# Optimization experiments

Hardware: AMD Instinct MI355X
Metric: run time of the kernel (lower is better)

## Reference

```python
import jax, jax.numpy as jnp
import numpy as np

D = 256
K = 3  # depthwise conv kernel size (odd)
A_EPS = 1e-4
POW_MIN = 1e-20
LN_EPS = 1e-5


def setup_inputs() -> dict:
    key = jax.random.key(0)
    ks = jax.random.split(key, 10)
    B, H, W = 8, 96, 96
    x = jax.random.normal(ks[0], (B, H, W, D), dtype=jnp.float32)
    inp = {
        'x': x,
        'ln_g': jnp.ones((D,), jnp.float32),
        'ln_b': jnp.zeros((D,), jnp.float32),
        'w_in': jax.random.normal(ks[1], (D, 2 * D), jnp.float32) * 0.02,
        'b_in': jnp.zeros((2 * D,), jnp.float32),
        'conv_w': jax.random.normal(ks[2], (K, K, 1, D), jnp.float32) * 0.1,
        'conv_b': jnp.zeros((D,), jnp.float32),
        'a_logit': 7.0 + 0.1 * jax.random.normal(ks[3], (D,), jnp.float32),
        'ssm_b': jnp.ones((D,), jnp.float32) + 0.02 * jax.random.normal(ks[4], (D,), jnp.float32),
        'ssm_c': jnp.ones((D,), jnp.float32) + 0.02 * jax.random.normal(ks[5], (D,), jnp.float32),
        'ssm_d': jnp.ones((D,), jnp.float32) + 0.02 * jax.random.normal(ks[6], (D,), jnp.float32),
        'w_out': jax.random.normal(ks[7], (D, D), jnp.float32) * 0.02,
        'b_out': jnp.zeros((D,), jnp.float32),
    }
    return inp


def _ssm_scan(x, a_logit, b, c, d):
    # x: (N, L, D). s_t = a*s_{t-1} + b*x_t ; y_t = c*s_t + d*x_t
    # via log-domain cumsum reformulation (as in the torch source).
    L = x.shape[1]
    a = jnp.clip(jax.nn.sigmoid(a_logit), A_EPS, 1.0 - A_EPS)  # (D,)
    t = jnp.arange(L, dtype=jnp.float32)
    a_pow = jnp.maximum(jnp.exp(t[:, None] * jnp.log(a)[None, :]), POW_MIN)  # (L,D)
    u = x * b  # (N,L,D)
    r = jnp.cumsum(u / a_pow[None], axis=1)
    return r * a_pow[None] * c + x * d


def reference(x, ln_g, ln_b, w_in, b_in, conv_w, conv_b,
              a_logit, ssm_b, ssm_c, ssm_d, w_out, b_out):
    B, H, W, Dm = x.shape
    x0 = x
    # LayerNorm over channel dim
    mu = jnp.mean(x, axis=-1, keepdims=True)
    var = jnp.mean(jnp.square(x - mu), axis=-1, keepdims=True)
    h = (x - mu) * jax.lax.rsqrt(var + LN_EPS) * ln_g + ln_b
    # in_proj -> split into value and gate
    xg = h @ w_in + b_in  # (B,H,W,2D)
    x_in, gate = jnp.split(xg, 2, axis=-1)
    gate = jax.nn.sigmoid(gate)
    # depthwise conv (SAME padding) + SiLU, NHWC layout
    u = jax.lax.conv_general_dilated(
        x_in, conv_w, window_strides=(1, 1), padding='SAME',
        dimension_numbers=('NHWC', 'HWIO', 'NHWC'), feature_group_count=Dm)
    u = jax.nn.silu(u + conv_b)
    # 2D bidirectional scan mixing
    L = H * W
    seq_row = u.reshape(B, L, Dm)
    seq_col = u.transpose(0, 2, 1, 3).reshape(B, L, Dm)

    def bid(s):
        yf = _ssm_scan(s, a_logit, ssm_b, ssm_c, ssm_d)
        yb = jnp.flip(_ssm_scan(jnp.flip(s, axis=1), a_logit, ssm_b, ssm_c, ssm_d), axis=1)
        return 0.5 * (yf + yb)

    y_row = bid(seq_row).reshape(B, H, W, Dm)
    y_col = bid(seq_col).reshape(B, W, H, Dm).transpose(0, 2, 1, 3)
    y = 0.5 * (y_row + y_col)
    # gate, out_proj, residual
    y = y * gate
    y = y @ w_out + b_out
    return x0 + y
```

## Files before the change

### kernel.cpp

```cpp
#include <hip/hip_runtime.h>
#include <math.h>

#define DD   256
#define HHH  96
#define WWW  96
#define NB   8
#define LL   9216
#define NPIX (NB*LL)
#define TCH  32
#define NCH  (LL/TCH)

typedef __bf16 bf16_8 __attribute__((ext_vector_type(8)));
typedef float  f32_4  __attribute__((ext_vector_type(4)));

static __device__ __forceinline__ float sigmoidf_(float x) {
    return 1.0f / (1.0f + expf(-x));
}

typedef const __attribute__((address_space(1))) void gas_void;
typedef __attribute__((address_space(3))) void las_void;
static __device__ __forceinline__ void glld16(const void* g, void* l) {
    __builtin_amdgcn_global_load_lds((gas_void*)g, (las_void*)l, 16, 0, 0);
}

template<int DIR>
static __device__ __forceinline__ int spidx(int t) {
    if (DIR == 0) return t;
    int w = t / HHH;
    int h = t - w * HHH;
    return h * WWW + w;
}

__global__ __launch_bounds__(256) void wcvt_kernel(const float* __restrict__ w_in,
                                                   const float* __restrict__ w_out,
                                                   __bf16* __restrict__ w_inT,
                                                   __bf16* __restrict__ w_outT) {
    int i = blockIdx.x * 256 + threadIdx.x;
    int n = i >> 8, k = i & 255;
    w_inT[i] = (__bf16)w_in[k * 512 + n];
    if (i < 256 * 256) w_outT[i] = (__bf16)w_out[k * 256 + n];
}

__global__ __launch_bounds__(256) void ln_kernel(const float* __restrict__ x,
                                                 const float* __restrict__ g,
                                                 const float* __restrict__ b,
                                                 __bf16* __restrict__ h) {
    int wv = threadIdx.x >> 6, lane = threadIdx.x & 63;
    int pix = blockIdx.x * 4 + wv;
    const float4 v = *(const float4*)&x[(size_t)pix * DD + lane * 4];
    float s  = v.x + v.y + v.z + v.w;
    float s2 = v.x * v.x + v.y * v.y + v.z * v.z + v.w * v.w;
    #pragma unroll
    for (int o = 32; o > 0; o >>= 1) {
        s  += __shfl_xor(s, o, 64);
        s2 += __shfl_xor(s2, o, 64);
    }
    float mu  = s * (1.0f / 256.0f);
    float var = s2 * (1.0f / 256.0f) - mu * mu;
    float r = rsqrtf(var + 1e-5f);
    float4 gg = *(const float4*)&g[lane * 4];
    float4 bb = *(const float4*)&b[lane * 4];
    union { ushort4 u; __bf16 e[4]; } o4;
    o4.e[0] = (__bf16)((v.x - mu) * r * gg.x + bb.x);
    o4.e[1] = (__bf16)((v.y - mu) * r * gg.y + bb.y);
    o4.e[2] = (__bf16)((v.z - mu) * r * gg.z + bb.z);
    o4.e[3] = (__bf16)((v.w - mu) * r * gg.w + bb.w);
    *(ushort4*)&h[(size_t)pix * DD + lane * 4] = o4.u;
}

template<int MODE>
__global__ __launch_bounds__(256) void gemm_bf16(const __bf16* __restrict__ A,
                                                 const __bf16* __restrict__ BT,
                                                 const float* __restrict__ bias,
                                                 __bf16* __restrict__ out_xin,
                                                 __bf16* __restrict__ out_gate,
                                                 float* __restrict__ out_f32,
                                                 const float* __restrict__ x0) {
    const int K = 256;
    const int BK = 32;
    __shared__ __bf16 As[2][128 * BK];
    __shared__ __bf16 Bs[2][128 * BK];
    int tid = threadIdx.x;
    int lane = tid & 63, wv = tid >> 6;
    int rowBase = blockIdx.x * 128;
    int colBase = blockIdx.y * 128;

    int srow = tid >> 2, sseg = tid & 3;
    const __bf16* aS0 = A  + (size_t)(rowBase + srow) * K + sseg * 8;
    const __bf16* aS1 = A  + (size_t)(rowBase + srow + 64) * K + sseg * 8;
    const __bf16* bS0 = BT + (size_t)(colBase + srow) * K + sseg * 8;
    const __bf16* bS1 = BT + (size_t)(colBase + srow + 64) * K + sseg * 8;
    int wvoff = wv * 1024;

    int m0 = (wv >> 1) * 64, n0 = (wv & 1) * 64;
    int fr = lane & 15, fq = lane >> 4;

    f32_4 acc[4][4];
    #pragma unroll
    for (int i = 0; i < 4; i++)
        #pragma unroll
        for (int j = 0; j < 4; j++) acc[i][j] = (f32_4){0.f, 0.f, 0.f, 0.f};

#define STAGE(bufi, koff)                                                  \
    do {                                                                   \
        glld16(aS0 + (koff), (char*)&As[bufi][0] + wvoff);                 \
        glld16(aS1 + (koff), (char*)&As[bufi][0] + 4096 + wvoff);          \
        glld16(bS0 + (koff), (char*)&Bs[bufi][0] + wvoff);                 \
        glld16(bS1 + (koff), (char*)&Bs[bufi][0] + 4096 + wvoff);          \
    } while (0)

    STAGE(0, 0);
    __syncthreads();
    int cur = 0;
    for (int t = 0; t < 8; ++t) {
        if (t < 7) STAGE(cur ^ 1, (t + 1) * BK);
        bf16_8 af[4], bb[4];
        #pragma unroll
        for (int mi = 0; mi < 4; mi++)
            af[mi] = *(const bf16_8*)&As[cur][(m0 + mi * 16 + fr) * BK + fq * 8];
        #pragma unroll
        for (int ni = 0; ni < 4; ni++)
            bb[ni] = *(const bf16_8*)&Bs[cur][(n0 + ni * 16 + fr) * BK + fq * 8];
        #pragma unroll
        for (int mi = 0; mi < 4; mi++)
            #pragma unroll
            for (int ni = 0; ni < 4; ni++)
                acc[mi][ni] = __builtin_amdgcn_mfma_f32_16x16x32_bf16(
                    af[mi], bb[ni], acc[mi][ni], 0, 0, 0);
        __syncthreads();
        cur ^= 1;
    }
#undef STAGE

    int rowW = rowBase + m0 + fq * 4;
    int colW = colBase + n0 + fr;
    #pragma unroll
    for (int mi = 0; mi < 4; mi++) {
        #pragma unroll
        for (int ni = 0; ni < 4; ni++) {
            int col = colW + ni * 16;
            float bv = bias[col];
            #pragma unroll
            for (int r = 0; r < 4; r++) {
                int row = rowW + mi * 16 + r;
                float v = acc[mi][ni][r] + bv;
                if (MODE == 0) {
                    if (col < 256) {
                        out_xin[(size_t)row * 256 + col] = (__bf16)v;
                    } else {
                        out_gate[(size_t)row * 256 + (col - 256)] = (__bf16)sigmoidf_(v);
                    }
                } else {
                    out_f32[(size_t)row * 256 + col] = v + x0[(size_t)row * 256 + col];
                }
            }
        }
    }
}

static __device__ __forceinline__ void loadcol(const __bf16* __restrict__ xin,
                                               int b, int h, int w, int d,
                                               float c[3]) {
    if (w < 0 || w >= WWW) { c[0] = c[1] = c[2] = 0.f; return; }
    size_t base = ((size_t)b * LL + (size_t)h * WWW + w) * DD + d;
    c[0] = (h > 0)       ? (float)xin[base - (size_t)WWW * DD] : 0.f;
    c[1] = (float)xin[base];
    c[2] = (h + 1 < HHH) ? (float)xin[base + (size_t)WWW * DD] : 0.f;
}

__global__ __launch_bounds__(256) void conv_tot_kernel(const __bf16* __restrict__ xin,
                                                       const float* __restrict__ cw,
                                                       const float* __restrict__ cb,
                                                       const float* __restrict__ a_logit,
                                                       const float* __restrict__ ssm_b,
                                                       __bf16* __restrict__ u,
                                                       float* __restrict__ tot_f,
                                                       float* __restrict__ tot_b) {
    int cx = blockIdx.x, h = blockIdx.y, b = blockIdx.z;
    int d = threadIdx.x;
    int w0 = cx * TCH;
    float k[9];
    #pragma unroll
    for (int i = 0; i < 9; i++) k[i] = cw[i * DD + d];
    float bias = cb[d];
    float a = sigmoidf_(a_logit[d]);
    a = fminf(fmaxf(a, 1e-4f), 1.0f - 1e-4f);
    float bb = ssm_b[d];

    float cl[3], cc[3], cr[3];
    loadcol(xin, b, h, w0 - 1, d, cl);
    loadcol(xin, b, h, w0,     d, cc);
    loadcol(xin, b, h, w0 + 1, d, cr);

    float v[TCH];
    float sf = 0.f;
    size_t outBase = ((size_t)b * LL + (size_t)h * WWW + w0) * DD + d;
    #pragma unroll
    for (int j = 0; j < TCH; j++) {
        float nx[3];
        loadcol(xin, b, h, w0 + j + 2, d, nx);
        float acc = bias;
        acc += k[0] * cl[0] + k[1] * cc[0] + k[2] * cr[0];
        acc += k[3] * cl[1] + k[4] * cc[1] + k[5] * cr[1];
        acc += k[6] * cl[2] + k[7] * cc[2] + k[8] * cr[2];
        float uv = acc * sigmoidf_(acc);
        v[j] = uv;
        u[outBase + (size_t)j * DD] = (__bf16)uv;
        sf = a * sf + bb * uv;
        cl[0] = cc[0]; cl[1] = cc[1]; cl[2] = cc[2];
        cc[0] = cr[0]; cc[1] = cr[1]; cc[2] = cr[2];
        cr[0] = nx[0]; cr[1] = nx[1]; cr[2] = nx[2];
    }
    int chunk = h * 3 + cx;
    tot_f[((size_t)b * NCH + chunk) * DD + d] = sf;
    float sb = 0.f;
    #pragma unroll
    for (int j = TCH - 1; j >= 0; j--) sb = a * sb + bb * v[j];
    tot_b[((size_t)b * NCH + chunk) * DD + d] = sb;
}

__global__ __launch_bounds__(256) void scan_totals_col(const __bf16* __restrict__ u,
                                                       const float* __restrict__ a_logit,
                                                       const float* __restrict__ ssm_b,
                                                       float* __restrict__ tot_f,
                                                       float* __restrict__ tot_b) {
    int blk = blockIdx.x;
    int b = blk / NCH, c = blk - b * NCH;
    int d = threadIdx.x;
    float a = sigmoidf_(a_logit[d]);
    a = fminf(fmaxf(a, 1e-4f), 1.0f - 1e-4f);
    float bb = ssm_b[d];
    size_t base = (size_t)b * LL * DD;
    int t0 = c * TCH;
    float v[TCH];
    #pragma unroll
    for (int j = 0; j < TCH; j++)
        v[j] = (float)u[base + (size_t)spidx<1>(t0 + j) * DD + d];
    float s = 0.f;
    #pragma unroll
    for (int j = 0; j < TCH; j++) s = a * s + bb * v[j];
    tot_f[(size_t)blk * DD + d] = s;
    s = 0.f;
    #pragma unroll
    for (int j = TCH - 1; j >= 0; j--) s = a * s + bb * v[j];
    tot_b[(size_t)blk * DD + d] = s;
}

__global__ __launch_bounds__(256) void scan_carries(const float* __restrict__ tot_all,
                                                    const float* __restrict__ a_logit,
                                                    float* __restrict__ car_all) {
    int b = blockIdx.x;
    int var = blockIdx.y;
    int d = threadIdx.x;
    float a = sigmoidf_(a_logit[d]);
    a = fminf(fmaxf(a, 1e-4f), 1.0f - 1e-4f);
    float a2 = a * a, a4 = a2 * a2, a8 = a4 * a4, a16 = a8 * a8;
    float q = a16 * a16;
    const float* tot = tot_all + (size_t)var * NB * NCH * DD + (size_t)b * NCH * DD + d;
    float* car = car_all + (size_t)var * NB * NCH * DD + (size_t)b * NCH * DD + d;
    float P = 0.f;
    if ((var & 1) == 0) {
        for (int c0 = 0; c0 < NCH; c0 += 8) {
            float t[8];
            #pragma unroll
            for (int j = 0; j < 8; j++) t[j] = tot[(size_t)(c0 + j) * DD];
            #pragma unroll
            for (int j = 0; j < 8; j++) {
                car[(size_t)(c0 + j) * DD] = P;
                P = q * P + t[j];
            }
        }
    } else {
        for (int c0 = NCH - 8; c0 >= 0; c0 -= 8) {
            float t[8];
            #pragma unroll
            for (int j = 0; j < 8; j++) t[j] = tot[(size_t)(c0 + j) * DD];
            #pragma unroll
            for (int j = 7; j >= 0; j--) {
                car[(size_t)(c0 + j) * DD] = P;
                P = q * P + t[j];
            }
        }
    }
}

template<int DIR>
__global__ __launch_bounds__(256) void scan_apply(const __bf16* __restrict__ u,
                                                  const float* __restrict__ a_logit,
                                                  const float* __restrict__ ssm_b,
                                                  const float* __restrict__ ssm_c,
                                                  const float* __restrict__ ssm_d,
                                                  const float* __restrict__ car_f,
                                                  const float* __restrict__ car_b,
                                                  float* __restrict__ y,
                                                  const __bf16* __restrict__ gate,
                                                  __bf16* __restrict__ g) {
    int blk = blockIdx.x;
    int b = blk / NCH, c = blk - b * NCH;
    int d = threadIdx.x;
    float a = sigmoidf_(a_logit[d]);
    a = fminf(fmaxf(a, 1e-4f), 1.0f - 1e-4f);
    float bb = ssm_b[d], cc = ssm_c[d], dd = ssm_d[d];
    size_t base = (size_t)b * LL * DD;
    int t0 = c * TCH;
    float v[TCH];
    #pragma unroll
    for (int j = 0; j < TCH; j++)
        v[j] = (float)u[base + (size_t)spidx<DIR>(t0 + j) * DD + d];
    float yf[TCH];
    float s = car_f[(size_t)blk * DD + d];
    #pragma unroll
    for (int j = 0; j < TCH; j++) {
        s = a * s + bb * v[j];
        yf[j] = cc * s + dd * v[j];
    }
    s = car_b[(size_t)blk * DD + d];
    #pragma unroll
    for (int j = TCH - 1; j >= 0; j--) {
        s = a * s + bb * v[j];
        float val = 0.25f * (yf[j] + cc * s + dd * v[j]);
        size_t idx = base + (size_t)spidx<DIR>(t0 + j) * DD + d;
        if (DIR == 0) {
            y[idx] = val;
        } else {
            float t = y[idx] + val;
            g[idx] = (__bf16)(t * (float)gate[idx]);
        }
    }
}

extern "C" void kernel_launch(void* const* d_in, const int* in_sizes, int n_in,
                              void* d_out, int out_size, void* d_ws, size_t ws_size,
                              hipStream_t stream) {
    const float* x       = (const float*)d_in[0];
    const float* ln_g    = (const float*)d_in[1];
    const float* ln_b    = (const float*)d_in[2];
    const float* w_in    = (const float*)d_in[3];
    const float* b_in    = (const float*)d_in[4];
    const float* conv_w  = (const float*)d_in[5];
    const float* conv_b  = (const float*)d_in[6];
    const float* a_logit = (const float*)d_in[7];
    const float* ssm_b   = (const float*)d_in[8];
    const float* ssm_c   = (const float*)d_in[9];
    const float* ssm_d   = (const float*)d_in[10];
    const float* w_out   = (const float*)d_in[11];
    const float* b_out   = (const float*)d_in[12];
    float* out = (float*)d_out;

    char* ws = (char*)d_ws;
    const size_t SZH = (size_t)NPIX * DD * sizeof(__bf16);
    const size_t TS  = (size_t)NB * NCH * DD * sizeof(float);

    __bf16* hB     = (__bf16*)(ws);
    __bf16* xinB   = (__bf16*)(ws + SZH);
    __bf16* uB     = (__bf16*)(ws + 2 * SZH);
    __bf16* gateB  = (__bf16*)(ws + 3 * SZH);
    float*  tot    = (float*)(ws + 4 * SZH);
    float*  car    = (float*)(ws + 4 * SZH + 4 * TS);
    __bf16* w_inT  = (__bf16*)(ws + 4 * SZH + 8 * TS);
    __bf16* w_outT = w_inT + 512 * 256;
    float* y = out;

    wcvt_kernel<<<512, 256, 0, stream>>>(w_in, w_out, w_inT, w_outT);
    ln_kernel<<<NPIX / 4, 256, 0, stream>>>(x, ln_g, ln_b, hB);
    gemm_bf16<0><<<dim3(NPIX / 128, 4), 256, 0, stream>>>(hB, w_inT, b_in,
                                                          xinB, gateB, nullptr, nullptr);
    conv_tot_kernel<<<dim3(WWW / TCH, HHH, NB), 256, 0, stream>>>(
        xinB, conv_w, conv_b, a_logit, ssm_b, uB,
        tot + 0 * (size_t)NB * NCH * DD, tot + 1 * (size_t)NB * NCH * DD);
    scan_totals_col<<<NB * NCH, 256, 0, stream>>>(
        uB, a_logit, ssm_b,
        tot + 2 * (size_t)NB * NCH * DD, tot + 3 * (size_t)NB * NCH * DD);
    scan_carries<<<dim3(NB, 4), 256, 0, stream>>>(tot, a_logit, car);
    scan_apply<0><<<NB * NCH, 256, 0, stream>>>(
        uB, a_logit, ssm_b, ssm_c, ssm_d,
        car + 0 * (size_t)NB * NCH * DD, car + 1 * (size_t)NB * NCH * DD,
        y, nullptr, nullptr);
    scan_apply<1><<<NB * NCH, 256, 0, stream>>>(
        uB, a_logit, ssm_b, ssm_c, ssm_d,
        car + 2 * (size_t)NB * NCH * DD, car + 3 * (size_t)NB * NCH * DD,
        y, gateB, hB);
    gemm_bf16<1><<<dim3(NPIX / 128, 2), 256, 0, stream>>>(hB, w_outT, b_out,
                                                          nullptr, nullptr, out, x);
}
```

Baseline: 410.8 us.

## Load full K panel into LDS upfront and prefetch residual in GEMM

The GEMM now issues async global-to-LDS loads for all eight K slices at once (128 KB of LDS), then runs the MFMA loop with one barrier instead of double-buffering with a barrier per slice. For the out-projection mode it also prefetches the residual x0 values into registers before compute so their latency overlaps the matrix math. The cost is far higher LDS use and register pressure, with launch bounds capped at one block per CU, so occupancy drops.

```diff
diff --git a/kernel.cpp b/kernel.cpp
--- a/kernel.cpp
+++ b/kernel.cpp
@@ -69,7 +69,7 @@
 }
 
 template<int MODE>
-__global__ __launch_bounds__(256) void gemm_bf16(const __bf16* __restrict__ A,
+__global__ __launch_bounds__(256, 1) void gemm_bf16(const __bf16* __restrict__ A,
                                                  const __bf16* __restrict__ BT,
                                                  const float* __restrict__ bias,
                                                  __bf16* __restrict__ out_xin,
@@ -78,8 +78,8 @@
                                                  const float* __restrict__ x0) {
     const int K = 256;
     const int BK = 32;
-    __shared__ __bf16 As[2][128 * BK];
-    __shared__ __bf16 Bs[2][128 * BK];
+    __shared__ __bf16 As[8][128 * BK];
+    __shared__ __bf16 Bs[8][128 * BK];
     int tid = threadIdx.x;
     int lane = tid & 63, wv = tid >> 6;
     int rowBase = blockIdx.x * 128;
@@ -94,6 +94,28 @@
 
     int m0 = (wv >> 1) * 64, n0 = (wv & 1) * 64;
     int fr = lane & 15, fq = lane >> 4;
+    int rowW = rowBase + m0 + fq * 4;
+    int colW = colBase + n0 + fr;
+
+    #pragma unroll
+    for (int t = 0; t < 8; ++t) {
+        glld16(aS0 + t * BK, (char*)&As[t][0] + wvoff);
+        glld16(aS1 + t * BK, (char*)&As[t][0] + 4096 + wvoff);
+        glld16(bS0 + t * BK, (char*)&Bs[t][0] + wvoff);
+        glld16(bS1 + t * BK, (char*)&Bs[t][0] + 4096 + wvoff);
+    }
+
+    float x0r[4][4][4];
+    if (MODE == 1) {
+        #pragma unroll
+        for (int mi = 0; mi < 4; mi++)
+            #pragma unroll
+            for (int ni = 0; ni < 4; ni++)
+                #pragma unroll
+                for (int r = 0; r < 4; r++)
+                    x0r[mi][ni][r] = x0[(size_t)(rowW + mi * 16 + r) * 256
+                                        + colW + ni * 16];
+    }
 
     f32_4 acc[4][4];
     #pragma unroll
@@ -101,39 +123,25 @@
         #pragma unroll
         for (int j = 0; j < 4; j++) acc[i][j] = (f32_4){0.f, 0.f, 0.f, 0.f};
 
-#define STAGE(bufi, koff)                                                  \
-    do {                                                                   \
-        glld16(aS0 + (koff), (char*)&As[bufi][0] + wvoff);                 \
-        glld16(aS1 + (koff), (char*)&As[bufi][0] + 4096 + wvoff);          \
-        glld16(bS0 + (koff), (char*)&Bs[bufi][0] + wvoff);                 \
-        glld16(bS1 + (koff), (char*)&Bs[bufi][0] + 4096 + wvoff);          \
-    } while (0)
-
-    STAGE(0, 0);
     __syncthreads();
-    int cur = 0;
-    for (int t = 0; t < 8; ++t) {
-        if (t < 7) STAGE(cur ^ 1, (t + 1) * BK);
+
+    #pragma unroll
+    for (int ks = 0; ks < 8; ++ks) {
         bf16_8 af[4], bb[4];
         #pragma unroll
         for (int mi = 0; mi < 4; mi++)
-            af[mi] = *(const bf16_8*)&As[cur][(m0 + mi * 16 + fr) * BK + fq * 8];
+            af[mi] = *(const bf16_8*)&As[ks][(m0 + mi * 16 + fr) * BK + fq * 8];
         #pragma unroll
         for (int ni = 0; ni < 4; ni++)
-            bb[ni] = *(const bf16_8*)&Bs[cur][(n0 + ni * 16 + fr) * BK + fq * 8];
+            bb[ni] = *(const bf16_8*)&Bs[ks][(n0 + ni * 16 + fr) * BK + fq * 8];
         #pragma unroll
         for (int mi = 0; mi < 4; mi++)
             #pragma unroll
             for (int ni = 0; ni < 4; ni++)
                 acc[mi][ni] = __builtin_amdgcn_mfma_f32_16x16x32_bf16(
                     af[mi], bb[ni], acc[mi][ni], 0, 0, 0);
-        __syncthreads();
-        cur ^= 1;
-    }
-#undef STAGE
-
-    int rowW = rowBase + m0 + fq * 4;
-    int colW = colBase + n0 + fr;
+    }
+
     #pragma unroll
     for (int mi = 0; mi < 4; mi++) {
         #pragma unroll
@@ -151,7 +159,7 @@
                         out_gate[(size_t)row * 256 + (col - 256)] = (__bf16)sigmoidf_(v);
                     }
                 } else {
-                    out_f32[(size_t)row * 256 + col] = v + x0[(size_t)row * 256 + col];
+                    out_f32[(size_t)row * 256 + col] = v + x0r[mi][ni][r];
                 }
             }
         }
```

New measurement: 407.7 us. No clear change (-0.8%).
